# Optimization experiments

Hardware: AMD Instinct MI355X
Metric: run time of the kernel (lower is better)

## Reference

```python
import jax, jax.numpy as jnp
import numpy as np

BBOX_POS_MAX = 1024.0
BN_EPS = 1e-5


def _bn_eval(x, g, b, rm, rv):
    # BatchNorm1d in eval mode: affine transform with running stats
    return g * (x - rm) * jax.lax.rsqrt(rv + BN_EPS) + b


def setup_inputs() -> dict:
    key = jax.random.key(0)
    ks = jax.random.split(key, 24)
    B, N, F = 32, 512, 1024
    E = 32768
    H1, H2, H3 = 512, 256, 128          # node_pred_hidden
    EH1, EH2 = 64, 64                   # edge_pred_hidden
    NC, EC = 8, 10                      # node/edge concept channels
    BC = 9                              # bbox_channels (4 bbox + 4 dir + 1 prio)
    s = 0.02
    inp = {
        'roi_features': jax.random.normal(ks[0], (B, N, F), jnp.float32),
        'batch_bboxes': jax.random.uniform(ks[1], (B, N, 4), jnp.float32) * BBOX_POS_MAX,
        'batch_directions': jax.random.uniform(ks[2], (B, N, 4), jnp.float32),
        'batch_priorities': jax.random.uniform(ks[3], (B, N), jnp.float32),
        'batch_edge_index': jax.random.randint(ks[4], (B, 2, E), 0, N, jnp.int32),
        # node_predictor params
        'np_w1': jax.random.normal(ks[5], (F, H1), jnp.float32) * s,
        'np_b1': jnp.zeros((H1,), jnp.float32),
        'bn1_g': jnp.ones((H1,), jnp.float32),
        'bn1_b': jnp.zeros((H1,), jnp.float32),
        'bn1_rm': jnp.zeros((H1,), jnp.float32),
        'bn1_rv': jnp.ones((H1,), jnp.float32),
        'np_w2': jax.random.normal(ks[6], (H1, H2), jnp.float32) * s,
        'np_b2': jnp.zeros((H2,), jnp.float32),
        'bn2_g': jnp.ones((H2,), jnp.float32),
        'bn2_b': jnp.zeros((H2,), jnp.float32),
        'bn2_rm': jnp.zeros((H2,), jnp.float32),
        'bn2_rv': jnp.ones((H2,), jnp.float32),
        'np_w3': jax.random.normal(ks[7], (H2, H3), jnp.float32) * s,
        'np_b3': jnp.zeros((H3,), jnp.float32),
        'ni_w': jax.random.normal(ks[8], (H3, NC), jnp.float32) * s,
        'ni_b': jnp.zeros((NC,), jnp.float32),
        # edge_predictor params (input dim = 2 * bbox_channels)
        'ep_w1': jax.random.normal(ks[9], (2 * BC, EH1), jnp.float32) * s,
        'ep_b1': jnp.zeros((EH1,), jnp.float32),
        'ep_w2': jax.random.normal(ks[10], (EH1, EH2), jnp.float32) * s,
        'ep_b2': jnp.zeros((EH2,), jnp.float32),
        'ei_w': jax.random.normal(ks[11], (EH2, EC), jnp.float32) * s,
        'ei_b': jnp.zeros((EC,), jnp.float32),
    }
    return inp


def reference(roi_features, batch_bboxes, batch_directions, batch_priorities,
              batch_edge_index,
              np_w1, np_b1, bn1_g, bn1_b, bn1_rm, bn1_rv,
              np_w2, np_b2, bn2_g, bn2_b, bn2_rm, bn2_rv,
              np_w3, np_b3, ni_w, ni_b,
              ep_w1, ep_b1, ep_w2, ep_b2, ei_w, ei_b):
    B, N, F = roi_features.shape
    # ---- node path: MLP (eval-mode BN, dropout = identity) + sigmoid interpreter
    x = roi_features.reshape(B * N, F)
    h = jax.nn.relu(_bn_eval(x @ np_w1 + np_b1, bn1_g, bn1_b, bn1_rm, bn1_rv))
    h = jax.nn.relu(_bn_eval(h @ np_w2 + np_b2, bn2_g, bn2_b, bn2_rm, bn2_rv))
    h = jax.nn.relu(h @ np_w3 + np_b3)
    node_concepts = jax.nn.sigmoid(h @ ni_w + ni_b).reshape(B, N, -1)
    # ---- edge path: per-batch gather of node attrs via edge_index, concat, MLP
    node_attr = jnp.concatenate(
        [batch_bboxes / BBOX_POS_MAX, batch_directions, batch_priorities[..., None]],
        axis=-1)  # [B, N, 9]
    C = node_attr.shape[-1]
    src_idx = batch_edge_index[:, 0, :, None]  # [B, E, 1]
    dst_idx = batch_edge_index[:, 1, :, None]
    src = jnp.take_along_axis(node_attr, src_idx.astype(jnp.int32), axis=1)  # [B, E, 9]
    dst = jnp.take_along_axis(node_attr, dst_idx.astype(jnp.int32), axis=1)
    edge_attr = jnp.concatenate([src, dst], axis=-1).reshape(-1, 2 * C)  # [B*E, 18]
    e = jax.nn.relu(edge_attr @ ep_w1 + ep_b1)
    e = jax.nn.relu(e @ ep_w2 + ep_b2)
    edge_concepts = jax.nn.sigmoid(e @ ei_w + ei_b)  # [B*E, EC]
    return node_concepts, edge_concepts
```

## Files before the change

### kernel.cpp

```cpp
#include <hip/hip_runtime.h>
#include <cstdint>
#include <cstddef>

#define BN_EPSF 1e-5f

constexpr int B_  = 32, N_ = 512, F_ = 1024, E_ = 32768;
constexpr int H1_ = 512, H2_ = 256, H3_ = 128, NC_ = 8, EC_ = 10;
constexpr int M_  = B_ * N_;
constexpr int NE_ = B_ * E_;

typedef short bf16x8 __attribute__((ext_vector_type(8)));
typedef float f32x4  __attribute__((ext_vector_type(4)));

__device__ __forceinline__ short f2bf(float f) {
  union { float f; unsigned u; } v; v.f = f;
  unsigned r = v.u + 0x7fffu + ((v.u >> 16) & 1u);
  return (short)(r >> 16);
}
__device__ __forceinline__ unsigned rnepack(float a, float b) {
  unsigned ua = __float_as_uint(a); ua = ua + 0x7fffu + ((ua >> 16) & 1u);
  unsigned ub = __float_as_uint(b); ub = ub + 0x7fffu + ((ub >> 16) & 1u);
  return __builtin_amdgcn_perm(ub, ua, 0x07060302u);
}

#define GLDS(gp, lp) __builtin_amdgcn_global_load_lds( \
    (const __attribute__((address_space(1))) void*)(gp), \
    (__attribute__((address_space(3))) void*)(lp), 16, 0, 0)

__device__ __forceinline__ void wt_body(
    const float* __restrict__ W, short* __restrict__ Wt, int K, int N,
    int bx, int by, float (*s)[33])
{
  const int tx = threadIdx.x & 31, ty = threadIdx.x >> 5;
  const int k0 = by * 32, n0 = bx * 32;
#pragma unroll
  for (int r = 0; r < 4; r++)
    s[ty * 4 + r][tx] = W[(size_t)(k0 + ty * 4 + r) * N + n0 + tx];
  __syncthreads();
#pragma unroll
  for (int r = 0; r < 4; r++)
    Wt[(size_t)(n0 + ty * 4 + r) * K + k0 + tx] = f2bf(s[tx][ty * 4 + r]);
}

__global__ __launch_bounds__(256) void k_prep(
    const float* __restrict__ roi, ushort* __restrict__ roiB,
    const float* __restrict__ w1, short* __restrict__ w1t,
    const float* __restrict__ w2, short* __restrict__ w2t,
    const float* __restrict__ w3, short* __restrict__ w3t,
    const float* __restrict__ bbox, const float* __restrict__ dir,
    const float* __restrict__ pri, float* __restrict__ na)
{
  __shared__ float s[32][33];
  const int bx = blockIdx.x;
  if (bx < 8192) {
    int i = bx * 256 + threadIdx.x;
    float4 a = *(const float4*)(roi + (size_t)i * 8);
    float4 b = *(const float4*)(roi + (size_t)i * 8 + 4);
    unsigned o[4];
    o[0] = rnepack(a.x, a.y); o[1] = rnepack(a.z, a.w);
    o[2] = rnepack(b.x, b.y); o[3] = rnepack(b.z, b.w);
    *(uint4*)(roiB + (size_t)i * 8) = *(uint4*)o;
  } else if (bx < 8704) {
    int idx = bx - 8192; wt_body(w1, w1t, F_, H1_, idx & 15, idx >> 4, s);
  } else if (bx < 8832) {
    int idx = bx - 8704; wt_body(w2, w2t, H1_, H2_, idx & 7, idx >> 3, s);
  } else if (bx < 8864) {
    int idx = bx - 8832; wt_body(w3, w3t, H2_, H3_, idx & 3, idx >> 2, s);
  } else {
    int i = (bx - 8864) * 256 + threadIdx.x;
    float4 b = *(const float4*)(bbox + (size_t)i * 4);
    float4 d = *(const float4*)(dir + (size_t)i * 4);
    float p = pri[i];
    const float inv = 1.0f / 1024.0f;
    float* o = na + (size_t)i * 12;
    *(float4*)(o + 0) = make_float4(b.x * inv, b.y * inv, b.z * inv, b.w * inv);
    *(float4*)(o + 4) = make_float4(d.x, d.y, d.z, d.w);
    *(float4*)(o + 8) = make_float4(p, 0.f, 0.f, 0.f);
  }
}

__global__ __launch_bounds__(256) void k_node_fused(
    const short* __restrict__ roiB, const short* __restrict__ w1t,
    const short* __restrict__ w2t, const short* __restrict__ w3t,
    const float* __restrict__ b1, const float* __restrict__ g1,
    const float* __restrict__ bb1, const float* __restrict__ rm1,
    const float* __restrict__ rv1,
    const float* __restrict__ b2, const float* __restrict__ g2,
    const float* __restrict__ bb2, const float* __restrict__ rm2,
    const float* __restrict__ rv2,
    const float* __restrict__ b3, const float* __restrict__ niw,
    const float* __restrict__ nib, float* __restrict__ out)
{
  __shared__ short sA[2 * 32 * 32];
  __shared__ short sStage[256 * 32];
  __shared__ short sH1c[32 * 136];
  __shared__ short sH2[32 * 264];

  const int tid  = threadIdx.x;
  const int wave = tid >> 6, lane = tid & 63;
  const int lm = lane & 15, q = lane >> 4;
  const int wm = wave >> 1, wn = wave & 1;
  const int m0 = blockIdx.x * 32;

  const int srow2 = tid >> 2;
  const int skq2  = (tid & 3) * 8;

  f32x4 acc2[8] = {};

  for (int n1 = 0; n1 < 4; n1++) {
    f32x4 acc1[4] = {};
    for (int k0 = 0; k0 < 1024; k0 += 64) {
      {
        int c = tid >> 7, row = (tid >> 2) & 31;
        GLDS(roiB + (size_t)(m0 + row) * 1024 + k0 + c * 32 + skq2,
             (char*)sA + wave * 1024);
      }
#pragma unroll
      for (int it = 0; it < 2; it++)
#pragma unroll
        for (int c = 0; c < 2; c++)
          GLDS(w1t + (size_t)(n1 * 128 + it * 64 + srow2) * 1024 + k0 + c * 32 + skq2,
               (char*)sStage + c * 8192 + it * 4096 + wave * 1024);
      __syncthreads();

      bf16x8 af[2];
      af[0] = *(const bf16x8*)&sA[(wm * 16 + lm) * 32 + q * 8];
      af[1] = *(const bf16x8*)&sA[1024 + (wm * 16 + lm) * 32 + q * 8];
#pragma unroll
      for (int nt = 0; nt < 4; nt++)
#pragma unroll
        for (int c = 0; c < 2; c++) {
          bf16x8 bfr = *(const bf16x8*)&sStage[c * 4096 + (wn * 64 + nt * 16 + lm) * 32 + q * 8];
          acc1[nt] = __builtin_amdgcn_mfma_f32_16x16x32_bf16(af[c], bfr, acc1[nt], 0, 0, 0);
        }
      __syncthreads();
    }
#pragma unroll
    for (int nt = 0; nt < 4; nt++) {
      int cl = wn * 64 + nt * 16 + lm;
      int col = n1 * 128 + cl;
      float s = g1[col] * rsqrtf(rv1[col] + BN_EPSF);
      float t = bb1[col] - rm1[col] * s;
      float bi = b1[col];
#pragma unroll
      for (int r = 0; r < 4; r++) {
        float v = fmaf(acc1[nt][r] + bi, s, t);
        sH1c[(wm * 16 + q * 4 + r) * 136 + cl] = f2bf(fmaxf(v, 0.f));
      }
    }
    __syncthreads();
    for (int kc = 0; kc < 4; kc++) {
#pragma unroll
      for (int it = 0; it < 4; it++)
        GLDS(w2t + (size_t)(it * 64 + srow2) * 512 + n1 * 128 + kc * 32 + skq2,
             (char*)sStage + it * 4096 + wave * 1024);
      __syncthreads();
      bf16x8 af2 = *(const bf16x8*)&sH1c[(wm * 16 + lm) * 136 + kc * 32 + q * 8];
#pragma unroll
      for (int nt = 0; nt < 8; nt++) {
        bf16x8 bfr = *(const bf16x8*)&sStage[(wn * 128 + nt * 16 + lm) * 32 + q * 8];
        acc2[nt] = __builtin_amdgcn_mfma_f32_16x16x32_bf16(af2, bfr, acc2[nt], 0, 0, 0);
      }
      __syncthreads();
    }
  }

#pragma unroll
  for (int nt = 0; nt < 8; nt++) {
    int col = wn * 128 + nt * 16 + lm;
    float s = g2[col] * rsqrtf(rv2[col] + BN_EPSF);
    float t = bb2[col] - rm2[col] * s;
    float bi = b2[col];
#pragma unroll
    for (int r = 0; r < 4; r++) {
      float v = fmaf(acc2[nt][r] + bi, s, t);
      sH2[(wm * 16 + q * 4 + r) * 264 + col] = f2bf(fmaxf(v, 0.f));
    }
  }
  __syncthreads();

  f32x4 acc3[4] = {};
  for (int k0 = 0; k0 < 256; k0 += 64) {
#pragma unroll
    for (int it = 0; it < 2; it++)
#pragma unroll
      for (int c = 0; c < 2; c++)
        GLDS(w3t + (size_t)(it * 64 + srow2) * 256 + k0 + c * 32 + skq2,
             (char*)sStage + c * 8192 + it * 4096 + wave * 1024);
    __syncthreads();
#pragma unroll
    for (int c = 0; c < 2; c++) {
      bf16x8 af3 = *(const bf16x8*)&sH2[(wm * 16 + lm) * 264 + k0 + c * 32 + q * 8];
#pragma unroll
      for (int nt = 0; nt < 4; nt++) {
        bf16x8 bfr = *(const bf16x8*)&sStage[c * 4096 + (wn * 64 + nt * 16 + lm) * 32 + q * 8];
        acc3[nt] = __builtin_amdgcn_mfma_f32_16x16x32_bf16(af3, bfr, acc3[nt], 0, 0, 0);
      }
    }
    __syncthreads();
  }
  short* sH3 = sH1c;
#pragma unroll
  for (int nt = 0; nt < 4; nt++) {
    int col = wn * 64 + nt * 16 + lm;
    float bi = b3[col];
#pragma unroll
    for (int r = 0; r < 4; r++) {
      float v = acc3[nt][r] + bi;
      sH3[(wm * 16 + q * 4 + r) * 136 + col] = f2bf(fmaxf(v, 0.f));
    }
  }
  __syncthreads();

  if (wave < 2) {
    f32x4 a4 = {};
#pragma unroll
    for (int c = 0; c < 4; c++) {
      ushort tmp[8];
#pragma unroll
      for (int j = 0; j < 8; j++) {
        int k = c * 32 + q * 8 + j;
        tmp[j] = (lm < 8) ? (ushort)f2bf(niw[k * 8 + lm]) : (ushort)0;
      }
      bf16x8 fw = *(bf16x8*)tmp;
      bf16x8 af4 = *(const bf16x8*)&sH3[(wave * 16 + lm) * 136 + c * 32 + q * 8];
      a4 = __builtin_amdgcn_mfma_f32_16x16x32_bf16(af4, fw, a4, 0, 0, 0);
    }
    if (lm < 8) {
      float bi = nib[lm];
#pragma unroll
      for (int r = 0; r < 4; r++) {
        float v = a4[r] + bi;
        out[(size_t)(m0 + wave * 16 + q * 4 + r) * 8 + lm] = 1.f / (1.f + __expf(-v));
      }
    }
  }
}

__global__ __launch_bounds__(256, 2) void k_edge_mfma(
    const float* __restrict__ na, const int* __restrict__ eidx,
    const float* __restrict__ w1, const float* __restrict__ b1,
    const float* __restrict__ w2, const float* __restrict__ b2,
    const float* __restrict__ wo, const float* __restrict__ bo,
    float* __restrict__ out)
{
  __shared__ __align__(16) short sA[9216];
  __shared__ __align__(16) short sH1[128 * 72];
  __shared__ float sB[144];

  const int tid  = threadIdx.x;
  const int wave = tid >> 6, lane = tid & 63;
  const int lm  = lane & 15;
  const int lk8 = (lane >> 4) * 8;
  const int lr  = (lane >> 4) * 4;

  short* sW1 = sA;
  short* sW2 = sA + 2048;
  short* sW3 = sA + 6144;
  short* sX  = sA;
  short* sH2 = sA;

  for (int i = tid; i < 2048; i += 256) {
    int n = i >> 5, k = i & 31;
    sW1[i] = (k < 18) ? f2bf(w1[k * 64 + n]) : (short)0;
  }
  for (int i = tid; i < 4096; i += 256) {
    int n = i >> 6, k = i & 63;
    sW2[i] = f2bf(w2[k * 64 + n]);
  }
  for (int i = tid; i < 1024; i += 256) {
    int n = i >> 6, k = i & 63;
    sW3[i] = (n < 10) ? f2bf(wo[k * 10 + n]) : (short)0;
  }
  if (tid < 64) { sB[tid] = b1[tid]; sB[64 + tid] = b2[tid]; }
  if (tid < 16) sB[128 + tid] = (tid < 10) ? bo[tid] : 0.f;
  __syncthreads();

  bf16x8 fW1[4], fW2[4][2], fW3[2];
#pragma unroll
  for (int t = 0; t < 4; t++)
    fW1[t] = *(const bf16x8*)&sW1[(t * 16 + lm) * 32 + lk8];
#pragma unroll
  for (int t = 0; t < 4; t++)
#pragma unroll
    for (int ks = 0; ks < 2; ks++)
      fW2[t][ks] = *(const bf16x8*)&sW2[(t * 16 + lm) * 64 + ks * 32 + lk8];
#pragma unroll
  for (int ks = 0; ks < 2; ks++)
    fW3[ks] = *(const bf16x8*)&sW3[lm * 64 + ks * 32 + lk8];
  float bias1v[4], bias2v[4];
#pragma unroll
  for (int t = 0; t < 4; t++) {
    bias1v[t] = sB[t * 16 + lm];
    bias2v[t] = sB[64 + t * 16 + lm];
  }
  const float biasOv = sB[128 + lm];
  __syncthreads();

  for (int bi = 0; bi < 8; bi++) {
    const int e0 = (blockIdx.x * 8 + bi) * 128;

    if (tid < 128) {
      int e = e0 + tid;
      int b = e >> 15, kk = e & (E_ - 1);
      const int* ei = eidx + (size_t)b * 2 * E_;
      int s = ei[kk], d = ei[E_ + kk];
      const float* ps = na + ((size_t)b * N_ + s) * 12;
      const float* pd = na + ((size_t)b * N_ + d) * 12;
      float4 a0 = *(const float4*)(ps);
      float4 a1 = *(const float4*)(ps + 4);
      float  a2 = ps[8];
      float4 c0 = *(const float4*)(pd);
      float4 c1 = *(const float4*)(pd + 4);
      float  c2 = pd[8];
      ushort xr[32];
      xr[0] = (ushort)f2bf(a0.x); xr[1] = (ushort)f2bf(a0.y);
      xr[2] = (ushort)f2bf(a0.z); xr[3] = (ushort)f2bf(a0.w);
      xr[4] = (ushort)f2bf(a1.x); xr[5] = (ushort)f2bf(a1.y);
      xr[6] = (ushort)f2bf(a1.z); xr[7] = (ushort)f2bf(a1.w);
      xr[8] = (ushort)f2bf(a2);
      xr[9]  = (ushort)f2bf(c0.x); xr[10] = (ushort)f2bf(c0.y);
      xr[11] = (ushort)f2bf(c0.z); xr[12] = (ushort)f2bf(c0.w);
      xr[13] = (ushort)f2bf(c1.x); xr[14] = (ushort)f2bf(c1.y);
      xr[15] = (ushort)f2bf(c1.z); xr[16] = (ushort)f2bf(c1.w);
      xr[17] = (ushort)f2bf(c2);
#pragma unroll
      for (int i = 18; i < 32; i++) xr[i] = 0;
      ushort* row = (ushort*)&sX[tid * 40];
      *(uint4*)(row + 0)  = *(uint4*)&xr[0];
      *(uint4*)(row + 8)  = *(uint4*)&xr[8];
      *(uint4*)(row + 16) = *(uint4*)&xr[16];
      *(uint4*)(row + 24) = *(uint4*)&xr[24];
    }
    __syncthreads();

    bf16x8 a1f[2];
#pragma unroll
    for (int ti = 0; ti < 2; ti++)
      a1f[ti] = *(const bf16x8*)&sX[(wave * 32 + ti * 16 + lm) * 40 + lk8];
    f32x4 acc1[2][4] = {};
#pragma unroll
    for (int ti = 0; ti < 2; ti++)
#pragma unroll
      for (int tj = 0; tj < 4; tj++)
        acc1[ti][tj] = __builtin_amdgcn_mfma_f32_16x16x32_bf16(
            a1f[ti], fW1[tj], acc1[ti][tj], 0, 0, 0);
#pragma unroll
    for (int ti = 0; ti < 2; ti++)
#pragma unroll
      for (int tj = 0; tj < 4; tj++)
#pragma unroll
        for (int r = 0; r < 4; r++) {
          int row = wave * 32 + ti * 16 + lr + r;
          float v = acc1[ti][tj][r] + bias1v[tj];
          sH1[row * 72 + tj * 16 + lm] = f2bf(fmaxf(v, 0.f));
        }
    __syncthreads();

    bf16x8 a2f[2][2];
#pragma unroll
    for (int ti = 0; ti < 2; ti++)
#pragma unroll
      for (int ks = 0; ks < 2; ks++)
        a2f[ti][ks] = *(const bf16x8*)&sH1[(wave * 32 + ti * 16 + lm) * 72 + ks * 32 + lk8];
    f32x4 acc2[2][4] = {};
#pragma unroll
    for (int ks = 0; ks < 2; ks++)
#pragma unroll
      for (int ti = 0; ti < 2; ti++)
#pragma unroll
        for (int tj = 0; tj < 4; tj++)
          acc2[ti][tj] = __builtin_amdgcn_mfma_f32_16x16x32_bf16(
              a2f[ti][ks], fW2[tj][ks], acc2[ti][tj], 0, 0, 0);
#pragma unroll
    for (int ti = 0; ti < 2; ti++)
#pragma unroll
      for (int tj = 0; tj < 4; tj++)
#pragma unroll
        for (int r = 0; r < 4; r++) {
          int row = wave * 32 + ti * 16 + lr + r;
          float v = acc2[ti][tj][r] + bias2v[tj];
          sH2[row * 72 + tj * 16 + lm] = f2bf(fmaxf(v, 0.f));
        }

    bf16x8 a3f[2][2];
#pragma unroll
    for (int ti = 0; ti < 2; ti++)
#pragma unroll
      for (int ks = 0; ks < 2; ks++)
        a3f[ti][ks] = *(const bf16x8*)&sH2[(wave * 32 + ti * 16 + lm) * 72 + ks * 32 + lk8];
    f32x4 acc3[2] = {};
#pragma unroll
    for (int ks = 0; ks < 2; ks++)
#pragma unroll
      for (int ti = 0; ti < 2; ti++)
        acc3[ti] = __builtin_amdgcn_mfma_f32_16x16x32_bf16(
            a3f[ti][ks], fW3[ks], acc3[ti], 0, 0, 0);
    if (lm < 10) {
#pragma unroll
      for (int ti = 0; ti < 2; ti++)
#pragma unroll
        for (int r = 0; r < 4; r++) {
          int row = wave * 32 + ti * 16 + lr + r;
          float v = acc3[ti][r] + biasOv;
          out[(size_t)(e0 + row) * 10 + lm] = 1.f / (1.f + __expf(-v));
        }
    }
    __syncthreads();
  }
}

extern "C" void kernel_launch(void* const* d_in, const int* in_sizes, int n_in,
                              void* d_out, int out_size, void* d_ws, size_t ws_size,
                              hipStream_t stream)
{
  const float* roi   = (const float*)d_in[0];
  const float* bbox  = (const float*)d_in[1];
  const float* dir   = (const float*)d_in[2];
  const float* pri   = (const float*)d_in[3];
  const int*   eidx  = (const int*)d_in[4];
  const float* w1    = (const float*)d_in[5];
  const float* b1    = (const float*)d_in[6];
  const float* g1    = (const float*)d_in[7];
  const float* bb1   = (const float*)d_in[8];
  const float* rm1   = (const float*)d_in[9];
  const float* rv1   = (const float*)d_in[10];
  const float* w2    = (const float*)d_in[11];
  const float* b2    = (const float*)d_in[12];
  const float* g2    = (const float*)d_in[13];
  const float* bb2   = (const float*)d_in[14];
  const float* rm2   = (const float*)d_in[15];
  const float* rv2   = (const float*)d_in[16];
  const float* w3    = (const float*)d_in[17];
  const float* b3    = (const float*)d_in[18];
  const float* niw   = (const float*)d_in[19];
  const float* nib   = (const float*)d_in[20];
  const float* ew1   = (const float*)d_in[21];
  const float* eb1   = (const float*)d_in[22];
  const float* ew2   = (const float*)d_in[23];
  const float* eb2   = (const float*)d_in[24];
  const float* eow   = (const float*)d_in[25];
  const float* eob   = (const float*)d_in[26];

  float* out_node = (float*)d_out;
  float* out_edge = (float*)d_out + (size_t)M_ * NC_;

  char* w = (char*)d_ws;
  short*  roiB = (short*)w;
  short*  w1t  = (short*)(w + 33554432);
  short*  w2t  = (short*)(w + 34603008);
  short*  w3t  = (short*)(w + 34865152);
  float*  na   = (float*)(w + 34930688);

  k_prep<<<8928, 256, 0, stream>>>(roi, (ushort*)roiB, w1, w1t, w2, w2t,
                                   w3, w3t, bbox, dir, pri, na);

  k_edge_mfma<<<NE_ / 1024, 256, 0, stream>>>(
      na, eidx, ew1, eb1, ew2, eb2, eow, eob, out_edge);

  k_node_fused<<<M_ / 32, 256, 0, stream>>>(
      roiB, w1t, w2t, w3t,
      b1, g1, bb1, rm1, rv1,
      b2, g2, bb2, rm2, rv2,
      b3, niw, nib, out_node);
}
```

Measured before the change: 274.5 us.

## Split node MLP into 128x128 tiled layer-1 GEMM and fused tail kernel

Replaces the single fused node kernel, which used 32-row tiles and re-streamed all of W1 for every block, with a separate 128x128-tile GEMM for the first layer that writes the bf16 H1 activations to workspace. A second kernel then runs layers 2-4 on 32-row tiles, reading H1 and the full W2 per k-step. The larger tile gives more operand reuse per LDS load in the dominant 1024x512 GEMM, at the cost of writing and re-reading H1 through global memory. Separately, the edge kernel now processes 4 sub-blocks per block instead of 8, doubling its grid.

```diff
diff --git a/kernel.cpp b/kernel.cpp
--- a/kernel.cpp
+++ b/kernel.cpp
@@ -26,6 +26,8 @@
 #define GLDS(gp, lp) __builtin_amdgcn_global_load_lds( \
     (const __attribute__((address_space(1))) void*)(gp), \
     (__attribute__((address_space(3))) void*)(lp), 16, 0, 0)
+
+#define MFMA(a, b, c) __builtin_amdgcn_mfma_f32_16x16x32_bf16((a), (b), (c), 0, 0, 0)
 
 __device__ __forceinline__ void wt_body(
     const float* __restrict__ W, short* __restrict__ Wt, int K, int N,
@@ -79,92 +81,119 @@
   }
 }
 
-__global__ __launch_bounds__(256) void k_node_fused(
-    const short* __restrict__ roiB, const short* __restrict__ w1t,
-    const short* __restrict__ w2t, const short* __restrict__ w3t,
-    const float* __restrict__ b1, const float* __restrict__ g1,
-    const float* __restrict__ bb1, const float* __restrict__ rm1,
-    const float* __restrict__ rv1,
+__global__ __launch_bounds__(256) void k_gemm_l1(
+    const short* __restrict__ A, const short* __restrict__ Wt,
+    const float* __restrict__ bias,
+    const float* __restrict__ g, const float* __restrict__ bb,
+    const float* __restrict__ rm, const float* __restrict__ rv,
+    short* __restrict__ C, int M, int K, int N)
+{
+  __shared__ short As[128 * 32];
+  __shared__ short Bs[128 * 32];
+
+  const int tid  = threadIdx.x;
+  const int wave = tid >> 6, lane = tid & 63;
+  const int m0 = blockIdx.y * 128, n0 = blockIdx.x * 128;
+  const int wm = wave >> 1, wn = wave & 1;
+
+  const int arow = tid >> 2;
+  const int akq  = (tid & 3) * 8;
+
+  f32x4 acc[4][4] = {};
+
+  for (int k0 = 0; k0 < K; k0 += 32) {
+#pragma unroll
+    for (int it = 0; it < 2; it++)
+      GLDS(A + (size_t)(m0 + it * 64 + arow) * K + k0 + akq,
+           (char*)As + it * 4096 + wave * 1024);
+#pragma unroll
+    for (int it = 0; it < 2; it++)
+      GLDS(Wt + (size_t)(n0 + it * 64 + arow) * K + k0 + akq,
+           (char*)Bs + it * 4096 + wave * 1024);
+    __syncthreads();
+
+    const int ko = (lane >> 4) * 8;
+    bf16x8 af[4], bfr[4];
+#pragma unroll
+    for (int t = 0; t < 4; t++) {
+      af[t]  = *(const bf16x8*)&As[(wm * 64 + t * 16 + (lane & 15)) * 32 + ko];
+      bfr[t] = *(const bf16x8*)&Bs[(wn * 64 + t * 16 + (lane & 15)) * 32 + ko];
+    }
+#pragma unroll
+    for (int ti = 0; ti < 4; ti++)
+#pragma unroll
+      for (int tj = 0; tj < 4; tj++)
+        acc[ti][tj] = MFMA(af[ti], bfr[tj], acc[ti][tj]);
+    __syncthreads();
+  }
+
+#pragma unroll
+  for (int tj = 0; tj < 4; tj++) {
+    const int col = n0 + wn * 64 + tj * 16 + (lane & 15);
+    const float bi = bias[col];
+    float s = g[col] * rsqrtf(rv[col] + BN_EPSF);
+    float t = bb[col] - rm[col] * s;
+#pragma unroll
+    for (int ti = 0; ti < 4; ti++) {
+      const int rbase = m0 + wm * 64 + ti * 16 + ((lane >> 4) << 2);
+#pragma unroll
+      for (int r = 0; r < 4; r++) {
+        float v = fmaf(acc[ti][tj][r] + bi, s, t);
+        C[(size_t)(rbase + r) * N + col] = f2bf(fmaxf(v, 0.f));
+      }
+    }
+  }
+}
+
+__global__ __launch_bounds__(256) void k_tail(
+    const short* __restrict__ h1, const short* __restrict__ w2t,
+    const short* __restrict__ w3t,
     const float* __restrict__ b2, const float* __restrict__ g2,
     const float* __restrict__ bb2, const float* __restrict__ rm2,
     const float* __restrict__ rv2,
     const float* __restrict__ b3, const float* __restrict__ niw,
     const float* __restrict__ nib, float* __restrict__ out)
 {
-  __shared__ short sA[2 * 32 * 32];
-  __shared__ short sStage[256 * 32];
-  __shared__ short sH1c[32 * 136];
-  __shared__ short sH2[32 * 264];
+  __shared__ __align__(16) char arena[53760];
+  short* sA  = (short*)arena;
+  short* sB  = (short*)(arena + 4096);
+  short* sH2 = (short*)(arena + 36864);
+  short* sB3 = (short*)arena;
+  short* sH3 = (short*)(arena + 16384);
 
   const int tid  = threadIdx.x;
   const int wave = tid >> 6, lane = tid & 63;
   const int lm = lane & 15, q = lane >> 4;
   const int wm = wave >> 1, wn = wave & 1;
   const int m0 = blockIdx.x * 32;
-
-  const int srow2 = tid >> 2;
-  const int skq2  = (tid & 3) * 8;
+  const int srow = tid >> 2;
+  const int skq  = (tid & 3) * 8;
 
   f32x4 acc2[8] = {};
-
-  for (int n1 = 0; n1 < 4; n1++) {
-    f32x4 acc1[4] = {};
-    for (int k0 = 0; k0 < 1024; k0 += 64) {
-      {
-        int c = tid >> 7, row = (tid >> 2) & 31;
-        GLDS(roiB + (size_t)(m0 + row) * 1024 + k0 + c * 32 + skq2,
-             (char*)sA + wave * 1024);
+  for (int k0 = 0; k0 < 512; k0 += 64) {
+    {
+      int c = tid >> 7, row = (tid >> 2) & 31;
+      GLDS(h1 + (size_t)(m0 + row) * 512 + k0 + c * 32 + skq,
+           (char*)sA + wave * 1024);
+    }
+#pragma unroll
+    for (int it = 0; it < 4; it++)
+#pragma unroll
+      for (int c = 0; c < 2; c++)
+        GLDS(w2t + (size_t)(it * 64 + srow) * 512 + k0 + c * 32 + skq,
+             (char*)sB + c * 16384 + it * 4096 + wave * 1024);
+    __syncthreads();
+#pragma unroll
+    for (int c = 0; c < 2; c++) {
+      bf16x8 af = *(const bf16x8*)&sA[c * 1024 + (wm * 16 + lm) * 32 + q * 8];
+#pragma unroll
+      for (int nt = 0; nt < 8; nt++) {
+        bf16x8 bfr = *(const bf16x8*)&sB[c * 8192 + (wn * 128 + nt * 16 + lm) * 32 + q * 8];
+        acc2[nt] = MFMA(af, bfr, acc2[nt]);
       }
-#pragma unroll
-      for (int it = 0; it < 2; it++)
-#pragma unroll
-        for (int c = 0; c < 2; c++)
-          GLDS(w1t + (size_t)(n1 * 128 + it * 64 + srow2) * 1024 + k0 + c * 32 + skq2,
-               (char*)sStage + c * 8192 + it * 4096 + wave * 1024);
-      __syncthreads();
-
-      bf16x8 af[2];
-      af[0] = *(const bf16x8*)&sA[(wm * 16 + lm) * 32 + q * 8];
-      af[1] = *(const bf16x8*)&sA[1024 + (wm * 16 + lm) * 32 + q * 8];
-#pragma unroll
-      for (int nt = 0; nt < 4; nt++)
-#pragma unroll
-        for (int c = 0; c < 2; c++) {
-          bf16x8 bfr = *(const bf16x8*)&sStage[c * 4096 + (wn * 64 + nt * 16 + lm) * 32 + q * 8];
-          acc1[nt] = __builtin_amdgcn_mfma_f32_16x16x32_bf16(af[c], bfr, acc1[nt], 0, 0, 0);
-        }
-      __syncthreads();
-    }
-#pragma unroll
-    for (int nt = 0; nt < 4; nt++) {
-      int cl = wn * 64 + nt * 16 + lm;
-      int col = n1 * 128 + cl;
-      float s = g1[col] * rsqrtf(rv1[col] + BN_EPSF);
-      float t = bb1[col] - rm1[col] * s;
-      float bi = b1[col];
-#pragma unroll
-      for (int r = 0; r < 4; r++) {
-        float v = fmaf(acc1[nt][r] + bi, s, t);
-        sH1c[(wm * 16 + q * 4 + r) * 136 + cl] = f2bf(fmaxf(v, 0.f));
-      }
-    }
-    __syncthreads();
-    for (int kc = 0; kc < 4; kc++) {
-#pragma unroll
-      for (int it = 0; it < 4; it++)
-        GLDS(w2t + (size_t)(it * 64 + srow2) * 512 + n1 * 128 + kc * 32 + skq2,
-             (char*)sStage + it * 4096 + wave * 1024);
-      __syncthreads();
-      bf16x8 af2 = *(const bf16x8*)&sH1c[(wm * 16 + lm) * 136 + kc * 32 + q * 8];
-#pragma unroll
-      for (int nt = 0; nt < 8; nt++) {
-        bf16x8 bfr = *(const bf16x8*)&sStage[(wn * 128 + nt * 16 + lm) * 32 + q * 8];
-        acc2[nt] = __builtin_amdgcn_mfma_f32_16x16x32_bf16(af2, bfr, acc2[nt], 0, 0, 0);
-      }
-      __syncthreads();
-    }
-  }
-
+    }
+    __syncthreads();
+  }
 #pragma unroll
   for (int nt = 0; nt < 8; nt++) {
     int col = wn * 128 + nt * 16 + lm;
@@ -185,21 +214,20 @@
     for (int it = 0; it < 2; it++)
 #pragma unroll
       for (int c = 0; c < 2; c++)
-        GLDS(w3t + (size_t)(it * 64 + srow2) * 256 + k0 + c * 32 + skq2,
-             (char*)sStage + c * 8192 + it * 4096 + wave * 1024);
+        GLDS(w3t + (size_t)(it * 64 + srow) * 256 + k0 + c * 32 + skq,
+             (char*)sB3 + c * 8192 + it * 4096 + wave * 1024);
     __syncthreads();
 #pragma unroll
     for (int c = 0; c < 2; c++) {
-      bf16x8 af3 = *(const bf16x8*)&sH2[(wm * 16 + lm) * 264 + k0 + c * 32 + q * 8];
+      bf16x8 af = *(const bf16x8*)&sH2[(wm * 16 + lm) * 264 + k0 + c * 32 + q * 8];
 #pragma unroll
       for (int nt = 0; nt < 4; nt++) {
-        bf16x8 bfr = *(const bf16x8*)&sStage[c * 4096 + (wn * 64 + nt * 16 + lm) * 32 + q * 8];
-        acc3[nt] = __builtin_amdgcn_mfma_f32_16x16x32_bf16(af3, bfr, acc3[nt], 0, 0, 0);
+        bf16x8 bfr = *(const bf16x8*)&sB3[c * 4096 + (wn * 64 + nt * 16 + lm) * 32 + q * 8];
+        acc3[nt] = MFMA(af, bfr, acc3[nt]);
       }
     }
     __syncthreads();
   }
-  short* sH3 = sH1c;
 #pragma unroll
   for (int nt = 0; nt < 4; nt++) {
     int col = wn * 64 + nt * 16 + lm;
@@ -224,7 +252,7 @@
       }
       bf16x8 fw = *(bf16x8*)tmp;
       bf16x8 af4 = *(const bf16x8*)&sH3[(wave * 16 + lm) * 136 + c * 32 + q * 8];
-      a4 = __builtin_amdgcn_mfma_f32_16x16x32_bf16(af4, fw, a4, 0, 0, 0);
+      a4 = MFMA(af4, fw, a4);
     }
     if (lm < 8) {
       float bi = nib[lm];
@@ -297,8 +325,8 @@
   const float biasOv = sB[128 + lm];
   __syncthreads();
 
-  for (int bi = 0; bi < 8; bi++) {
-    const int e0 = (blockIdx.x * 8 + bi) * 128;
+  for (int bi = 0; bi < 4; bi++) {
+    const int e0 = (blockIdx.x * 4 + bi) * 128;
 
     if (tid < 128) {
       int e = e0 + tid;
@@ -343,8 +371,7 @@
     for (int ti = 0; ti < 2; ti++)
 #pragma unroll
       for (int tj = 0; tj < 4; tj++)
-        acc1[ti][tj] = __builtin_amdgcn_mfma_f32_16x16x32_bf16(
-            a1f[ti], fW1[tj], acc1[ti][tj], 0, 0, 0);
+        acc1[ti][tj] = MFMA(a1f[ti], fW1[tj], acc1[ti][tj]);
 #pragma unroll
     for (int ti = 0; ti < 2; ti++)
 #pragma unroll
@@ -370,8 +397,7 @@
       for (int ti = 0; ti < 2; ti++)
 #pragma unroll
         for (int tj = 0; tj < 4; tj++)
-          acc2[ti][tj] = __builtin_amdgcn_mfma_f32_16x16x32_bf16(
-              a2f[ti][ks], fW2[tj][ks], acc2[ti][tj], 0, 0, 0);
+          acc2[ti][tj] = MFMA(a2f[ti][ks], fW2[tj][ks], acc2[ti][tj]);
 #pragma unroll
     for (int ti = 0; ti < 2; ti++)
 #pragma unroll
@@ -394,8 +420,7 @@
     for (int ks = 0; ks < 2; ks++)
 #pragma unroll
       for (int ti = 0; ti < 2; ti++)
-        acc3[ti] = __builtin_amdgcn_mfma_f32_16x16x32_bf16(
-            a3f[ti][ks], fW3[ks], acc3[ti], 0, 0, 0);
+        acc3[ti] = MFMA(a3f[ti][ks], fW3[ks], acc3[ti]);
     if (lm < 10) {
 #pragma unroll
       for (int ti = 0; ti < 2; ti++)
@@ -451,16 +476,16 @@
   short*  w2t  = (short*)(w + 34603008);
   short*  w3t  = (short*)(w + 34865152);
   float*  na   = (float*)(w + 34930688);
+  short*  h1   = (short*)(w + 35717120);
 
   k_prep<<<8928, 256, 0, stream>>>(roi, (ushort*)roiB, w1, w1t, w2, w2t,
                                    w3, w3t, bbox, dir, pri, na);
 
-  k_edge_mfma<<<NE_ / 1024, 256, 0, stream>>>(
+  k_edge_mfma<<<NE_ / 512, 256, 0, stream>>>(
       na, eidx, ew1, eb1, ew2, eb2, eow, eob, out_edge);
 
-  k_node_fused<<<M_ / 32, 256, 0, stream>>>(
-      roiB, w1t, w2t, w3t,
-      b1, g1, bb1, rm1, rv1,
-      b2, g2, bb2, rm2, rv2,
-      b3, niw, nib, out_node);
-}
+  k_gemm_l1<<<dim3(H1_ / 128, M_ / 128), 256, 0, stream>>>(
+      roiB, w1t, b1, g1, bb1, rm1, rv1, h1, M_, F_, H1_);
+  k_tail<<<M_ / 32, 256, 0, stream>>>(
+      h1, w2t, w3t, b2, g2, bb2, rm2, rv2, b3, niw, nib, out_node);
+}
```

Measured after the change: 267.8 us. -2.5%, faster.
